# Kernel optimization log

Hardware: AMD Instinct MI355X
Metric: run time of the kernel (lower is better)

The kernel has to match this reference:

```python
import jax, jax.numpy as jnp
import numpy as np

BS, N, HID, INPUT, PREK, KHOP = 16, 1024, 64, 64, 4, 3
D = 2 * HID            # hidden channel dim (128)
F = 2 * INPUT          # input feature dim (128)
C = F + D              # graphconv input channels (256)
NM = KHOP + 1          # num_metrics = k_hop*n_supports + 1 with n_supports=1
PI = 3.141592653589793
EMB_RANGE = (12.0 + 2.0) / HID   # (gamma + epsilon) / hidden_size


def setup_inputs() -> dict:
    key = jax.random.key(0)
    ks = jax.random.split(key, 12)
    inputs = jax.random.normal(ks[0], (BS, N, F), jnp.float32)
    # per-sample dynamic support; scale by 1/N to keep Chebyshev recursion stable
    supports = jax.random.uniform(ks[1], (BS, N, N), jnp.float32) / N
    hidden_states = jax.random.normal(ks[2], (BS, PREK, N, D), jnp.float32)
    W = jax.random.normal(ks[3], (D, D), jnp.float32) * 0.02
    b = jax.random.normal(ks[4], (N, D), jnp.float32) * 0.02
    R = jax.random.normal(ks[5], (PREK, N, HID), jnp.float32) * 0.02
    gc_w = jax.random.normal(ks[6], (D, C * NM), jnp.float32) * 0.02
    gc_b = jax.random.normal(ks[7], (D,), jnp.float32) * 0.02
    ev_att_w = jax.random.normal(ks[8], (1, N * D), jnp.float32) * 0.001
    ev_att_b = jax.random.normal(ks[9], (1,), jnp.float32) * 0.02
    att_w = jax.random.normal(ks[10], (1, N * D), jnp.float32) * 0.001
    att_b = jax.random.normal(ks[11], (1,), jnp.float32) * 0.02
    return {"inputs": inputs, "supports": supports, "hidden_states": hidden_states,
            "W": W, "b": b, "R": R, "gc_w": gc_w, "gc_b": gc_b,
            "ev_att_w": ev_att_w, "ev_att_b": ev_att_b,
            "att_w": att_w, "att_b": att_b}


def reference(inputs, supports, hidden_states, W, b, R, gc_w, gc_b,
              ev_att_w, ev_att_b, att_w, att_b):
    bs, k, n, d = hidden_states.shape
    # split inputs / last hidden into real/imag halves
    re_in, im_in = jnp.split(inputs, 2, axis=-1)          # [bs,n,INPUT]
    preH = hidden_states[:, -1]                           # [bs,n,d]
    re_p, im_p = jnp.split(preH, 2, axis=-1)              # [bs,n,HID]
    conv_in = jnp.concatenate([re_in, re_p, im_in, im_p], axis=-1)  # [bs,n,C]

    # diffusion graph conv (Chebyshev-style recursion over single batched support)
    x0 = conv_in
    x1 = jnp.matmul(supports, x0)                         # [bs,n,C]
    xs = [x0, x1]
    for _ in range(2, KHOP + 1):
        x2 = 2.0 * jnp.matmul(supports, x1) - x0
        xs.append(x2)
        x0, x1 = x1, x2
    # stack K metrics, permute to [bs,n,C,K], flatten (channel-major, step-minor)
    x = jnp.stack(xs, axis=0).transpose(1, 2, 3, 0).reshape(bs, n, C * NM)
    gco = x @ gc_w.T + gc_b                               # [bs,n,d]

    # EvolutionCell attention over g=1 group (kept for faithfulness)
    xe = gco.reshape(bs, 1, n * d)
    se = xe @ ev_att_w.T + ev_att_b                       # [bs,1,1]
    we = jax.nn.softmax(se, axis=1)
    conv_out = (xe * we).sum(axis=1).reshape(bs, n, d)

    # leaky_relu_ (slope 0.01)
    conv_out = jnp.where(conv_out >= 0, conv_out, 0.01 * conv_out)

    # RotatE-style complex phase rotation of hidden states
    phase = R / (EMB_RANGE / PI)                          # [k,n,HID]
    re_rel, im_rel = jnp.cos(phase), jnp.sin(phase)
    re_h, im_h = jnp.split(hidden_states, 2, axis=-1)     # [bs,k,n,HID]
    re_new = re_rel * re_h - im_rel * im_h
    im_new = im_rel * re_h + re_rel * im_h
    new_states = jnp.concatenate([re_new, im_new], axis=-1)  # [bs,k,n,d]

    # attention over k memory slots
    xa = new_states.reshape(bs, k, n * d)
    sa = xa @ att_w.T + att_b                             # [bs,k,1]
    wa = jax.nn.softmax(sa, axis=1)
    att = (xa * wa).sum(axis=1).reshape(bs, n, d)

    output = conv_out @ W + b[None] + att                 # [bs,n,d]
    new_hidden = jnp.concatenate([hidden_states[:, 1:], output[:, None]], axis=1)
    return output, new_hidden
```

## Files before the change

kernel.cpp:

```cpp
#include <hip/hip_runtime.h>
#include <cstddef>

constexpr float PHASE_SCALE = (float)(3.141592653589793 / ((12.0 + 2.0) / 64.0));

typedef __bf16 bf16;
typedef __bf16 bf16x4 __attribute__((ext_vector_type(4)));
typedef __bf16 bf16x8 __attribute__((ext_vector_type(8)));
typedef float floatx4 __attribute__((ext_vector_type(4)));

#define GLOAD_LDS16(gp, lp) __builtin_amdgcn_global_load_lds( \
    (const __attribute__((address_space(1))) void*)(gp),      \
    (__attribute__((address_space(3))) void*)(lp), 16, 0, 0)

#define VM_WAIT(n) asm volatile("s_waitcnt vmcnt(" #n ")" ::: "memory")

__global__ __launch_bounds__(256) void prep_misc(
    const float* __restrict__ R,
    const float* __restrict__ gcw, const float* __restrict__ W,
    bf16* __restrict__ gtAll, bf16* __restrict__ WT,
    const float* __restrict__ inp, const float* __restrict__ hs,
    bf16* __restrict__ xRow, bf16* __restrict__ xT0,
    const float* __restrict__ attw, float* __restrict__ part)
{
    __shared__ bf16 tile[64][65];
    __shared__ float red[256];
    const int bid = blockIdx.x;
    const int tid = threadIdx.x;

    if (bid < 576) {
        int gi = bid * 256 + tid;
        if (gi < 131072) {
            int m = gi >> 15;
            int rem = gi & 32767;
            int d = rem >> 8;
            int c = rem & 255;
            gtAll[gi] = (bf16)gcw[(size_t)d * 1024 + c * 4 + m];
        } else {
            int r = gi - 131072;
            int n = r >> 7, k = r & 127;
            WT[r] = (bf16)W[(size_t)k * 128 + n];
        }
    } else if (bid < 1088) {
        int bid3 = bid - 576;
        int bk = bid3 & 63;
        int k = bk & 3;
        int chunk = bid3 >> 6;
        const float* hbase = hs + (size_t)bk * 131072;
        float acc = 0.f;
        for (int idx = tid; idx < 2048; idx += 256) {
            int h4 = (idx & 15) * 4;
            int n = chunk * 128 + (idx >> 4);
            float4 rr  = *(const float4*)(R + (size_t)k * 65536 + n * 64 + h4);
            float4 re  = *(const float4*)(hbase + (size_t)n * 128 + h4);
            float4 im  = *(const float4*)(hbase + (size_t)n * 128 + 64 + h4);
            float4 wre = *(const float4*)(attw + (size_t)n * 128 + h4);
            float4 wim = *(const float4*)(attw + (size_t)n * 128 + 64 + h4);
            float sv, cv;
            __sincosf(rr.x * PHASE_SCALE, &sv, &cv);
            acc += (cv * re.x - sv * im.x) * wre.x + (sv * re.x + cv * im.x) * wim.x;
            __sincosf(rr.y * PHASE_SCALE, &sv, &cv);
            acc += (cv * re.y - sv * im.y) * wre.y + (sv * re.y + cv * im.y) * wim.y;
            __sincosf(rr.z * PHASE_SCALE, &sv, &cv);
            acc += (cv * re.z - sv * im.z) * wre.z + (sv * re.z + cv * im.z) * wim.z;
            __sincosf(rr.w * PHASE_SCALE, &sv, &cv);
            acc += (cv * re.w - sv * im.w) * wre.w + (sv * re.w + cv * im.w) * wim.w;
        }
        red[tid] = acc;
        __syncthreads();
        for (int s2 = 128; s2 > 0; s2 >>= 1) {
            if (tid < s2) red[tid] += red[tid + s2];
            __syncthreads();
        }
        if (tid == 0) part[bk * 8 + chunk] = red[0];
    } else {
        int lin = bid - 1088;
        int b = lin >> 6, by = (lin >> 2) & 15, bx = lin & 3;
        int n0 = by * 64, c0 = bx * 64;
        const float* base = (bx & 1) ? (hs + (((size_t)b * 4 + 3) * 1024) * 128)
                                     : (inp + ((size_t)b * 1024) * 128);
        int soff = (bx >> 1) * 64;
        #pragma unroll
        for (int it = 0; it < 2; ++it) {
            int unit = it * 256 + tid;
            int nl = unit >> 3, cs = unit & 7;
            const float* src = base + (size_t)(n0 + nl) * 128 + soff + cs * 8;
            float4 a0 = *(const float4*)src;
            float4 a1 = *(const float4*)(src + 4);
            bf16x8 o;
            o[0] = (bf16)a0.x; o[1] = (bf16)a0.y; o[2] = (bf16)a0.z; o[3] = (bf16)a0.w;
            o[4] = (bf16)a1.x; o[5] = (bf16)a1.y; o[6] = (bf16)a1.z; o[7] = (bf16)a1.w;
            *(bf16x8*)(xRow + ((size_t)b * 1024 + n0 + nl) * 256 + c0 + cs * 8) = o;
            #pragma unroll
            for (int e = 0; e < 8; ++e) tile[nl][cs * 8 + e] = o[e];
        }
        __syncthreads();
        #pragma unroll
        for (int it = 0; it < 4; ++it) {
            int unit = it * 256 + tid;
            int ng = unit & 15, cc = unit >> 4;
            bf16x4 v;
            #pragma unroll
            for (int r = 0; r < 4; ++r) v[r] = tile[ng * 4 + r][cc];
            *(bf16x4*)(xT0 + ((size_t)b * 256 + c0 + cc) * 1024 + n0 + ng * 4) = v;
        }
    }
}

__global__ __launch_bounds__(256) void sconv_kernel(
    const float4* __restrict__ S, bf16* __restrict__ Sbf)
{
    size_t t = (size_t)blockIdx.x * 512 + threadIdx.x;
    const float4* p0 = S + t * 2;
    const float4* p1 = S + (t + 256) * 2;
    float4 a0 = p0[0];
    float4 a1 = p0[1];
    float4 b0 = p1[0];
    float4 b1 = p1[1];
    bf16x8 oa, ob;
    oa[0] = (bf16)a0.x; oa[1] = (bf16)a0.y; oa[2] = (bf16)a0.z; oa[3] = (bf16)a0.w;
    oa[4] = (bf16)a1.x; oa[5] = (bf16)a1.y; oa[6] = (bf16)a1.z; oa[7] = (bf16)a1.w;
    ob[0] = (bf16)b0.x; ob[1] = (bf16)b0.y; ob[2] = (bf16)b0.z; ob[3] = (bf16)b0.w;
    ob[4] = (bf16)b1.x; ob[5] = (bf16)b1.y; ob[6] = (bf16)b1.z; ob[7] = (bf16)b1.w;
    *(bf16x8*)(Sbf + t * 8) = oa;
    *(bf16x8*)(Sbf + (t + 256) * 8) = ob;
}

__global__ __launch_bounds__(512) void cheb_mfma_kernel(
    const bf16* __restrict__ S, const bf16* __restrict__ xT,
    const bf16* __restrict__ xTprev, bf16* __restrict__ outT,
    const bf16* __restrict__ xRow0, const bf16* __restrict__ gtA,
    const bf16* __restrict__ gt0, float* __restrict__ gcoF,
    float alpha, int accumulate)
{
    __shared__ char smem[122880];
    const int f = blockIdx.x;
    const int b = (f & 7) + 8 * ((f >> 3) & 1);
    const int n0 = (f >> 4) * 64;
    const int tid = threadIdx.x;
    const int wave = tid >> 6, lane = tid & 63;
    const int wr = (wave & 3) * 16;
    const int wc = (wave >> 2) * 128;
    const int l15 = lane & 15, quad = lane >> 4;
    const int lrow = lane >> 3;
    const int segsw = (lane & 7) ^ lrow;

    const bf16* Sb = S + (size_t)b * 1048576;
    const bf16* xb = xT + (size_t)b * 262144;

    auto stage = [&](int buf, int k0) {
        bf16* dA = (bf16*)(smem + buf * 40960);
        bf16* dB = dA + 4096;
        {
            const bf16* gp = Sb + (size_t)(n0 + wave * 8 + lrow) * 1024 + k0 + segsw * 8;
            GLOAD_LDS16(gp, dA + wave * 8 * 64);
        }
        #pragma unroll
        for (int v = 0; v < 4; ++v) {
            int cq = wave * 32 + v * 8;
            const bf16* gp = xb + (size_t)(cq + lrow) * 1024 + k0 + segsw * 8;
            GLOAD_LDS16(gp, dB + cq * 64);
        }
    };

    floatx4 acc[8] = {};
    stage(0, 0);
    stage(1, 64);
    for (int i = 0; i < 16; ++i) {
        if (i < 15) { VM_WAIT(5); } else { VM_WAIT(0); }
        __builtin_amdgcn_s_barrier();
        __builtin_amdgcn_sched_barrier(0);
        const bf16* lA = (const bf16*)(smem + (i % 3) * 40960);
        const bf16* lB = lA + 4096;
        #pragma unroll
        for (int ks = 0; ks < 2; ++ks) {
            int row = wr + l15;
            int aslot = (ks * 4 + quad) ^ (row & 7);
            bf16x8 af = *(const bf16x8*)(lA + row * 64 + aslot * 8);
            #pragma unroll
            for (int j = 0; j < 8; ++j) {
                int col = wc + j * 16 + l15;
                int bslot = (ks * 4 + quad) ^ (col & 7);
                bf16x8 bfr = *(const bf16x8*)(lB + col * 64 + bslot * 8);
                acc[j] = __builtin_amdgcn_mfma_f32_16x16x32_bf16(af, bfr, acc[j], 0, 0, 0);
            }
        }
        if (i + 2 < 16) stage((i + 2) % 3, (i + 2) * 64);
    }

    const bf16* pT = xTprev ? xTprev + (size_t)b * 262144 : nullptr;
    bf16* oT = outT ? outT + (size_t)b * 262144 : nullptr;
    bf16x4 xo[8];
    #pragma unroll
    for (int j = 0; j < 8; ++j) {
        int col = wc + j * 16 + l15;
        float v[4];
        #pragma unroll
        for (int r = 0; r < 4; ++r) v[r] = alpha * acc[j][r];
        if (pT) {
            bf16x4 pp = *(const bf16x4*)(pT + (size_t)col * 1024 + n0 + wr + quad * 4);
            #pragma unroll
            for (int r = 0; r < 4; ++r) v[r] -= (float)pp[r];
        }
        #pragma unroll
        for (int r = 0; r < 4; ++r) xo[j][r] = (bf16)v[r];
        if (oT) *(bf16x4*)(oT + (size_t)col * 1024 + n0 + wr + quad * 4) = xo[j];
    }

    __syncthreads();
    bf16* ldsX = (bf16*)smem;
    #pragma unroll
    for (int j = 0; j < 8; ++j) {
        int col = wc + j * 16 + l15;
        #pragma unroll
        for (int r = 0; r < 4; ++r)
            ldsX[(wr + quad * 4 + r) * 264 + col] = xo[j][r];
    }
    __syncthreads();

    const int dbase = (wave >> 2) * 64;
    floatx4 a2[4] = {};
    for (int k2 = 0; k2 < 256; k2 += 32) {
        bf16x8 af = *(const bf16x8*)(ldsX + (wr + l15) * 264 + k2 + quad * 8);
        #pragma unroll
        for (int j = 0; j < 4; ++j) {
            int dcol = dbase + j * 16 + l15;
            bf16x8 bfr = *(const bf16x8*)(gtA + (size_t)dcol * 256 + k2 + quad * 8);
            a2[j] = __builtin_amdgcn_mfma_f32_16x16x32_bf16(af, bfr, a2[j], 0, 0, 0);
        }
    }
    if (xRow0) {
        for (int k2 = 0; k2 < 256; k2 += 32) {
            bf16x8 af = *(const bf16x8*)(xRow0 + ((size_t)b * 1024 + n0 + wr + l15) * 256 + k2 + quad * 8);
            #pragma unroll
            for (int j = 0; j < 4; ++j) {
                int dcol = dbase + j * 16 + l15;
                bf16x8 bfr = *(const bf16x8*)(gt0 + (size_t)dcol * 256 + k2 + quad * 8);
                a2[j] = __builtin_amdgcn_mfma_f32_16x16x32_bf16(af, bfr, a2[j], 0, 0, 0);
            }
        }
    }
    #pragma unroll
    for (int j = 0; j < 4; ++j) {
        int dcol = dbase + j * 16 + l15;
        #pragma unroll
        for (int r = 0; r < 4; ++r) {
            size_t idx = ((size_t)b * 1024 + n0 + wr + quad * 4 + r) * 128 + dcol;
            if (accumulate) gcoF[idx] += a2[j][r];
            else            gcoF[idx]  = a2[j][r];
        }
    }
}

__global__ __launch_bounds__(256) void final_kernel(
    const float* __restrict__ gcoF, const float* __restrict__ gcb,
    const bf16* __restrict__ WT, const float* __restrict__ bvec,
    const float* __restrict__ hs, const float* __restrict__ R,
    const float* __restrict__ part, const float* __restrict__ attb,
    float* __restrict__ out, float* __restrict__ newh)
{
    const int m0 = blockIdx.x * 64;
    const int b = m0 >> 10, n0 = m0 & 1023;
    const int tid = threadIdx.x;
    const int wave = tid >> 6, lane = tid & 63;
    const int l15 = lane & 15, quad = lane >> 4;

    const int arow = m0 + wave * 16 + l15;
    floatx4 acc[8] = {};
    #pragma unroll
    for (int k0 = 0; k0 < 128; k0 += 32) {
        int kk = k0 + quad * 8;
        float4 p0 = *(const float4*)(gcoF + (size_t)arow * 128 + kk);
        float4 p1 = *(const float4*)(gcoF + (size_t)arow * 128 + kk + 4);
        float4 g0 = *(const float4*)(gcb + kk);
        float4 g1 = *(const float4*)(gcb + kk + 4);
        float vv[8] = {p0.x + g0.x, p0.y + g0.y, p0.z + g0.z, p0.w + g0.w,
                       p1.x + g1.x, p1.y + g1.y, p1.z + g1.z, p1.w + g1.w};
        bf16x8 af;
        #pragma unroll
        for (int e = 0; e < 8; ++e) {
            float v = vv[e];
            af[e] = (bf16)(v >= 0.f ? v : 0.01f * v);
        }
        #pragma unroll
        for (int j = 0; j < 8; ++j) {
            bf16x8 bfr = *(const bf16x8*)(WT + (size_t)(j * 16 + l15) * 128 + kk);
            acc[j] = __builtin_amdgcn_mfma_f32_16x16x32_bf16(af, bfr, acc[j], 0, 0, 0);
        }
    }

    float sa[4], mx = -1e30f;
    #pragma unroll
    for (int k = 0; k < 4; ++k) {
        float s = attb[0];
        #pragma unroll
        for (int c = 0; c < 8; ++c) s += part[(b * 4 + k) * 8 + c];
        sa[k] = s;
        mx = fmaxf(mx, s);
    }
    float den = 0.f;
    #pragma unroll
    for (int k = 0; k < 4; ++k) { sa[k] = __expf(sa[k] - mx); den += sa[k]; }
    float inv = 1.f / den;
    #pragma unroll
    for (int k = 0; k < 4; ++k) sa[k] *= inv;

    #pragma unroll
    for (int jj = 0; jj < 4; ++jj) {
        int hcol = jj * 16 + l15;
        #pragma unroll
        for (int r = 0; r < 4; ++r) {
            int n = n0 + wave * 16 + quad * 4 + r;
            float attRe = 0.f, attIm = 0.f;
            #pragma unroll
            for (int k = 0; k < 4; ++k) {
                const float* hb = hs + (((size_t)(b * 4 + k) * 1024 + n) * 128);
                float re = hb[hcol], im = hb[64 + hcol];
                float s, c;
                __sincosf(R[(size_t)k * 65536 + n * 64 + hcol] * PHASE_SCALE, &s, &c);
                attRe += sa[k] * (c * re - s * im);
                attIm += sa[k] * (s * re + c * im);
                if (k >= 1) {
                    size_t nb = (size_t)b * 524288 + (size_t)(k - 1) * 131072 + (size_t)n * 128;
                    newh[nb + hcol] = re;
                    newh[nb + 64 + hcol] = im;
                }
            }
            size_t ob = (size_t)(m0 + wave * 16 + quad * 4 + r) * 128;
            float oRe = acc[jj][r]     + bvec[(size_t)n * 128 + hcol]      + attRe;
            float oIm = acc[jj + 4][r] + bvec[(size_t)n * 128 + 64 + hcol] + attIm;
            out[ob + hcol] = oRe;
            out[ob + 64 + hcol] = oIm;
            size_t nb3 = (size_t)b * 524288 + 393216 + (size_t)n * 128;
            newh[nb3 + hcol] = oRe;
            newh[nb3 + 64 + hcol] = oIm;
        }
    }
}

extern "C" void kernel_launch(void* const* d_in, const int* in_sizes, int n_in,
                              void* d_out, int out_size, void* d_ws, size_t ws_size,
                              hipStream_t stream) {
    const float* inp  = (const float*)d_in[0];
    const float* sup  = (const float*)d_in[1];
    const float* hs   = (const float*)d_in[2];
    const float* W    = (const float*)d_in[3];
    const float* bvec = (const float*)d_in[4];
    const float* R    = (const float*)d_in[5];
    const float* gcw  = (const float*)d_in[6];
    const float* gcb  = (const float*)d_in[7];
    const float* attw = (const float*)d_in[10];
    const float* attb = (const float*)d_in[11];

    float* out  = (float*)d_out;
    float* newh = out + 2097152;
    bf16*  Sbf  = (bf16*)newh;

    char* w = (char*)d_ws;
    bf16*  xT0   = (bf16*)(w);
    bf16*  xT1   = (bf16*)(w + 8388608);
    bf16*  xT2   = (bf16*)(w + 16777216);
    bf16*  xRow  = (bf16*)(w + 25165824);
    float* gcoF  = (float*)(w + 33554432);
    bf16*  gtAll = (bf16*)(w + 41943040);
    bf16*  WT    = (bf16*)(w + 42205184);
    float* part  = (float*)(w + 42237952);

    prep_misc<<<2112, 256, 0, stream>>>(R, gcw, W, gtAll, WT, inp, hs,
                                        xRow, xT0, attw, part);
    sconv_kernel<<<4096, 256, 0, stream>>>((const float4*)sup, Sbf);

    cheb_mfma_kernel<<<256, 512, 0, stream>>>(Sbf, xT0, nullptr, xT1,
                                              xRow, gtAll + 32768, gtAll, gcoF, 1.0f, 0);
    cheb_mfma_kernel<<<256, 512, 0, stream>>>(Sbf, xT1, xT0, xT2,
                                              nullptr, gtAll + 2 * 32768, nullptr, gcoF, 2.0f, 1);
    cheb_mfma_kernel<<<256, 512, 0, stream>>>(Sbf, xT2, xT1, nullptr,
                                              nullptr, gtAll + 3 * 32768, nullptr, gcoF, 2.0f, 1);

    final_kernel<<<256, 256, 0, stream>>>(gcoF, gcb, WT, bvec, hs, R, part, attb, out, newh);
}
```

Measured before the change: 266.8 us.

## Fuse three Chebyshev hop launches into one cooperative kernel with grid sync

Merges the three per-hop cheb_mfma_kernel launches into a single cooperative kernel that loops over hops and uses grid.sync between them. This is meant to remove kernel launch gaps and tail effects between dependent hops. The cost is grid-wide barrier overhead, a 256-block cooperative-launch requirement that must fit co-resident, and a possible loss of cross-hop cache benefits or compiler register pressure changes.

```diff
diff --git a/kernel.cpp b/kernel.cpp
--- a/kernel.cpp
+++ b/kernel.cpp
@@ -1,5 +1,8 @@
 #include <hip/hip_runtime.h>
+#include <hip/hip_cooperative_groups.h>
 #include <cstddef>
+
+namespace cg = cooperative_groups;
 
 constexpr float PHASE_SCALE = (float)(3.141592653589793 / ((12.0 + 2.0) / 64.0));
 
@@ -125,12 +128,11 @@
     *(bf16x8*)(Sbf + (t + 256) * 8) = ob;
 }
 
-__global__ __launch_bounds__(512) void cheb_mfma_kernel(
-    const bf16* __restrict__ S, const bf16* __restrict__ xT,
-    const bf16* __restrict__ xTprev, bf16* __restrict__ outT,
-    const bf16* __restrict__ xRow0, const bf16* __restrict__ gtA,
-    const bf16* __restrict__ gt0, float* __restrict__ gcoF,
-    float alpha, int accumulate)
+__global__ __launch_bounds__(512) void cheb3_kernel(
+    const bf16* __restrict__ S, const bf16* __restrict__ xT0,
+    bf16* __restrict__ xT1, bf16* __restrict__ xT2,
+    const bf16* __restrict__ xRow, const bf16* __restrict__ gtAll,
+    float* __restrict__ gcoF)
 {
     __shared__ char smem[122880];
     const int f = blockIdx.x;
@@ -145,108 +147,124 @@
     const int segsw = (lane & 7) ^ lrow;
 
     const bf16* Sb = S + (size_t)b * 1048576;
-    const bf16* xb = xT + (size_t)b * 262144;
-
-    auto stage = [&](int buf, int k0) {
-        bf16* dA = (bf16*)(smem + buf * 40960);
-        bf16* dB = dA + 4096;
-        {
-            const bf16* gp = Sb + (size_t)(n0 + wave * 8 + lrow) * 1024 + k0 + segsw * 8;
-            GLOAD_LDS16(gp, dA + wave * 8 * 64);
-        }
-        #pragma unroll
-        for (int v = 0; v < 4; ++v) {
-            int cq = wave * 32 + v * 8;
-            const bf16* gp = xb + (size_t)(cq + lrow) * 1024 + k0 + segsw * 8;
-            GLOAD_LDS16(gp, dB + cq * 64);
-        }
-    };
-
-    floatx4 acc[8] = {};
-    stage(0, 0);
-    stage(1, 64);
-    for (int i = 0; i < 16; ++i) {
-        if (i < 15) { VM_WAIT(5); } else { VM_WAIT(0); }
-        __builtin_amdgcn_s_barrier();
-        __builtin_amdgcn_sched_barrier(0);
-        const bf16* lA = (const bf16*)(smem + (i % 3) * 40960);
-        const bf16* lB = lA + 4096;
-        #pragma unroll
-        for (int ks = 0; ks < 2; ++ks) {
-            int row = wr + l15;
-            int aslot = (ks * 4 + quad) ^ (row & 7);
-            bf16x8 af = *(const bf16x8*)(lA + row * 64 + aslot * 8);
-            #pragma unroll
-            for (int j = 0; j < 8; ++j) {
-                int col = wc + j * 16 + l15;
-                int bslot = (ks * 4 + quad) ^ (col & 7);
-                bf16x8 bfr = *(const bf16x8*)(lB + col * 64 + bslot * 8);
-                acc[j] = __builtin_amdgcn_mfma_f32_16x16x32_bf16(af, bfr, acc[j], 0, 0, 0);
-            }
-        }
-        if (i + 2 < 16) stage((i + 2) % 3, (i + 2) * 64);
-    }
-
-    const bf16* pT = xTprev ? xTprev + (size_t)b * 262144 : nullptr;
-    bf16* oT = outT ? outT + (size_t)b * 262144 : nullptr;
-    bf16x4 xo[8];
-    #pragma unroll
-    for (int j = 0; j < 8; ++j) {
-        int col = wc + j * 16 + l15;
-        float v[4];
-        #pragma unroll
-        for (int r = 0; r < 4; ++r) v[r] = alpha * acc[j][r];
-        if (pT) {
-            bf16x4 pp = *(const bf16x4*)(pT + (size_t)col * 1024 + n0 + wr + quad * 4);
-            #pragma unroll
-            for (int r = 0; r < 4; ++r) v[r] -= (float)pp[r];
-        }
-        #pragma unroll
-        for (int r = 0; r < 4; ++r) xo[j][r] = (bf16)v[r];
-        if (oT) *(bf16x4*)(oT + (size_t)col * 1024 + n0 + wr + quad * 4) = xo[j];
-    }
-
-    __syncthreads();
-    bf16* ldsX = (bf16*)smem;
-    #pragma unroll
-    for (int j = 0; j < 8; ++j) {
-        int col = wc + j * 16 + l15;
-        #pragma unroll
-        for (int r = 0; r < 4; ++r)
-            ldsX[(wr + quad * 4 + r) * 264 + col] = xo[j][r];
-    }
-    __syncthreads();
-
-    const int dbase = (wave >> 2) * 64;
-    floatx4 a2[4] = {};
-    for (int k2 = 0; k2 < 256; k2 += 32) {
-        bf16x8 af = *(const bf16x8*)(ldsX + (wr + l15) * 264 + k2 + quad * 8);
+    cg::grid_group grid = cg::this_grid();
+
+    #pragma unroll 1
+    for (int hop = 0; hop < 3; ++hop) {
+        const bf16* xin   = (hop == 0) ? xT0 : (hop == 1) ? xT1 : xT2;
+        const bf16* xprev = (hop == 0) ? (const bf16*)nullptr : (hop == 1) ? xT0 : xT1;
+        bf16*       xout  = (hop == 0) ? xT1 : (hop == 1) ? xT2 : nullptr;
+        const bf16* gtA   = gtAll + (size_t)(hop + 1) * 32768;
+        const float alpha = (hop == 0) ? 1.0f : 2.0f;
+
+        const bf16* xb = xin + (size_t)b * 262144;
+
+        auto stage = [&](int buf, int k0) {
+            bf16* dA = (bf16*)(smem + buf * 40960);
+            bf16* dB = dA + 4096;
+            {
+                const bf16* gp = Sb + (size_t)(n0 + wave * 8 + lrow) * 1024 + k0 + segsw * 8;
+                GLOAD_LDS16(gp, dA + wave * 8 * 64);
+            }
+            #pragma unroll
+            for (int v = 0; v < 4; ++v) {
+                int cq = wave * 32 + v * 8;
+                const bf16* gp = xb + (size_t)(cq + lrow) * 1024 + k0 + segsw * 8;
+                GLOAD_LDS16(gp, dB + cq * 64);
+            }
+        };
+
+        floatx4 acc[8] = {};
+        stage(0, 0);
+        stage(1, 64);
+        for (int i = 0; i < 16; ++i) {
+            if (i < 15) { VM_WAIT(5); } else { VM_WAIT(0); }
+            __builtin_amdgcn_s_barrier();
+            __builtin_amdgcn_sched_barrier(0);
+            const bf16* lA = (const bf16*)(smem + (i % 3) * 40960);
+            const bf16* lB = lA + 4096;
+            #pragma unroll
+            for (int ks = 0; ks < 2; ++ks) {
+                int row = wr + l15;
+                int aslot = (ks * 4 + quad) ^ (row & 7);
+                bf16x8 af = *(const bf16x8*)(lA + row * 64 + aslot * 8);
+                #pragma unroll
+                for (int j = 0; j < 8; ++j) {
+                    int col = wc + j * 16 + l15;
+                    int bslot = (ks * 4 + quad) ^ (col & 7);
+                    bf16x8 bfr = *(const bf16x8*)(lB + col * 64 + bslot * 8);
+                    acc[j] = __builtin_amdgcn_mfma_f32_16x16x32_bf16(af, bfr, acc[j], 0, 0, 0);
+                }
+            }
+            if (i + 2 < 16) stage((i + 2) % 3, (i + 2) * 64);
+        }
+
+        const bf16* pT = xprev ? xprev + (size_t)b * 262144 : nullptr;
+        bf16* oT = xout ? xout + (size_t)b * 262144 : nullptr;
+        bf16x4 xo[8];
+        #pragma unroll
+        for (int j = 0; j < 8; ++j) {
+            int col = wc + j * 16 + l15;
+            float v[4];
+            #pragma unroll
+            for (int r = 0; r < 4; ++r) v[r] = alpha * acc[j][r];
+            if (pT) {
+                bf16x4 pp = *(const bf16x4*)(pT + (size_t)col * 1024 + n0 + wr + quad * 4);
+                #pragma unroll
+                for (int r = 0; r < 4; ++r) v[r] -= (float)pp[r];
+            }
+            #pragma unroll
+            for (int r = 0; r < 4; ++r) xo[j][r] = (bf16)v[r];
+            if (oT) *(bf16x4*)(oT + (size_t)col * 1024 + n0 + wr + quad * 4) = xo[j];
+        }
+
+        __syncthreads();
+        bf16* ldsX = (bf16*)smem;
+        #pragma unroll
+        for (int j = 0; j < 8; ++j) {
+            int col = wc + j * 16 + l15;
+            #pragma unroll
+            for (int r = 0; r < 4; ++r)
+                ldsX[(wr + quad * 4 + r) * 264 + col] = xo[j][r];
+        }
+        __syncthreads();
+
+        const int dbase = (wave >> 2) * 64;
+        floatx4 a2[4] = {};
+        for (int k2 = 0; k2 < 256; k2 += 32) {
+            bf16x8 af = *(const bf16x8*)(ldsX + (wr + l15) * 264 + k2 + quad * 8);
+            #pragma unroll
+            for (int j = 0; j < 4; ++j) {
+                int dcol = dbase + j * 16 + l15;
+                bf16x8 bfr = *(const bf16x8*)(gtA + (size_t)dcol * 256 + k2 + quad * 8);
+                a2[j] = __builtin_amdgcn_mfma_f32_16x16x32_bf16(af, bfr, a2[j], 0, 0, 0);
+            }
+        }
+        if (hop == 0) {
+            for (int k2 = 0; k2 < 256; k2 += 32) {
+                bf16x8 af = *(const bf16x8*)(xRow + ((size_t)b * 1024 + n0 + wr + l15) * 256 + k2 + quad * 8);
+                #pragma unroll
+                for (int j = 0; j < 4; ++j) {
+                    int dcol = dbase + j * 16 + l15;
+                    bf16x8 bfr = *(const bf16x8*)(gtAll + (size_t)dcol * 256 + k2 + quad * 8);
+                    a2[j] = __builtin_amdgcn_mfma_f32_16x16x32_bf16(af, bfr, a2[j], 0, 0, 0);
+                }
+            }
+        }
         #pragma unroll
         for (int j = 0; j < 4; ++j) {
             int dcol = dbase + j * 16 + l15;
-            bf16x8 bfr = *(const bf16x8*)(gtA + (size_t)dcol * 256 + k2 + quad * 8);
-            a2[j] = __builtin_amdgcn_mfma_f32_16x16x32_bf16(af, bfr, a2[j], 0, 0, 0);
-        }
-    }
-    if (xRow0) {
-        for (int k2 = 0; k2 < 256; k2 += 32) {
-            bf16x8 af = *(const bf16x8*)(xRow0 + ((size_t)b * 1024 + n0 + wr + l15) * 256 + k2 + quad * 8);
-            #pragma unroll
-            for (int j = 0; j < 4; ++j) {
-                int dcol = dbase + j * 16 + l15;
-                bf16x8 bfr = *(const bf16x8*)(gt0 + (size_t)dcol * 256 + k2 + quad * 8);
-                a2[j] = __builtin_amdgcn_mfma_f32_16x16x32_bf16(af, bfr, a2[j], 0, 0, 0);
-            }
-        }
-    }
-    #pragma unroll
-    for (int j = 0; j < 4; ++j) {
-        int dcol = dbase + j * 16 + l15;
-        #pragma unroll
-        for (int r = 0; r < 4; ++r) {
-            size_t idx = ((size_t)b * 1024 + n0 + wr + quad * 4 + r) * 128 + dcol;
-            if (accumulate) gcoF[idx] += a2[j][r];
-            else            gcoF[idx]  = a2[j][r];
+            #pragma unroll
+            for (int r = 0; r < 4; ++r) {
+                size_t idx = ((size_t)b * 1024 + n0 + wr + quad * 4 + r) * 128 + dcol;
+                if (hop) gcoF[idx] += a2[j][r];
+                else     gcoF[idx]  = a2[j][r];
+            }
+        }
+
+        if (hop < 2) {
+            __threadfence();
+            grid.sync();
         }
     }
 }
@@ -369,12 +387,19 @@
                                         xRow, xT0, attw, part);
     sconv_kernel<<<4096, 256, 0, stream>>>((const float4*)sup, Sbf);
 
-    cheb_mfma_kernel<<<256, 512, 0, stream>>>(Sbf, xT0, nullptr, xT1,
-                                              xRow, gtAll + 32768, gtAll, gcoF, 1.0f, 0);
-    cheb_mfma_kernel<<<256, 512, 0, stream>>>(Sbf, xT1, xT0, xT2,
-                                              nullptr, gtAll + 2 * 32768, nullptr, gcoF, 2.0f, 1);
-    cheb_mfma_kernel<<<256, 512, 0, stream>>>(Sbf, xT2, xT1, nullptr,
-                                              nullptr, gtAll + 3 * 32768, nullptr, gcoF, 2.0f, 1);
+    {
+        const bf16* SbfC  = Sbf;
+        const bf16* xT0C  = xT0;
+        bf16*       xT1P  = xT1;
+        bf16*       xT2P  = xT2;
+        const bf16* xRowC = xRow;
+        const bf16* gtC   = gtAll;
+        float*      gcoP  = gcoF;
+        void* args[] = {(void*)&SbfC, (void*)&xT0C, (void*)&xT1P, (void*)&xT2P,
+                        (void*)&xRowC, (void*)&gtC, (void*)&gcoP};
+        hipLaunchCooperativeKernel((void*)cheb3_kernel, dim3(256), dim3(512),
+                                   args, 0, stream);
+    }
 
     final_kernel<<<256, 256, 0, stream>>>(gcoF, gcb, WT, bvec, hs, R, part, attb, out, newh);
 }
```

New measurement: 451.9 us. 1.69x slower.
